# Kernel tuning notes

Hardware: AMD Instinct MI355X
Metric: run time of the kernel (lower is better)

Reference implementation:

```python
import jax, jax.numpy as jnp
from jax import lax
import numpy as np

B = 128          # batch size
S = 207          # input spatial size implied by outputSpatialSize=[8,8]
N_PTS = 256000
NEG = -1e30      # -inf stand-in for masked max-pooling
# BNReLU channel counts in execution order: 8 resnet blocks x (bn1, bn2), final resnet BN(32), last BN(64)
SIZES = [8,8,8,8,8,16,16,16,16,24,24,24,24,32,32,32,32,64]
OFF = np.cumsum([0] + SIZES)

WSHAPES = dict(conv0=(3,3,1,8),
               c1a=(3,3,8,8), c1b=(3,3,8,8), c2a=(3,3,8,8), c2b=(3,3,8,8),
               c3a=(3,3,8,16), c3b=(3,3,16,16), c3r=(3,3,8,16),
               c4a=(3,3,16,16), c4b=(3,3,16,16),
               c5a=(3,3,16,24), c5b=(3,3,24,24), c5r=(3,3,16,24),
               c6a=(3,3,24,24), c6b=(3,3,24,24),
               c7a=(3,3,24,32), c7b=(3,3,32,32), c7r=(3,3,24,32),
               c8a=(3,3,32,32), c8b=(3,3,32,32),
               conv_last=(5,5,32,64))

def _conv(x, w, stride, padding):
    return lax.conv_general_dilated(x, w, (stride, stride), padding,
                                    dimension_numbers=('NHWC', 'HWIO', 'NHWC'))

def _pool_max(x, win, stride, init):
    return lax.reduce_window(x, init, lax.max, (1, win, win, 1), (1, stride, stride, 1), 'VALID')

def _bnrelu(x, m, g, b):
    # eval-mode BN folded to affine, applied on active sites only (inactive stay exactly 0)
    return m * jax.nn.relu(x * g + b)

def _subconv(x, w, m):
    # submanifold conv == dense conv on zero-filled grid, output restricted to active sites
    return _conv(x, w, 1, 'SAME') * m

def _strided(x, w, m, win, stride):
    # scn.Convolution: output site active iff any active input in its receptive field
    m2 = _pool_max(m, win, stride, 0.0)
    return _conv(x, w, stride, 'VALID') * m2, m2

def _block(x, m, g1, b1, w1, g2, b2, w2, wres, stride):
    # pre-activation basic block from scn.SparseResNet
    h = _bnrelu(x, m, g1, b1)
    if stride == 1:
        h, m2 = _subconv(h, w1, m), m
    else:
        h, m2 = _strided(h, w1, m, 3, 2)
    h = _subconv(_bnrelu(h, m2, g2, b2), w2, m2)
    r = x if wres is None else _strided(x, wres, m, 3, 2)[0]
    return h + r, m2

def _forward(locations, batch_idx, features, bn_gamma, bn_beta, W):
    idx = (batch_idx, locations[:, 0], locations[:, 1], jnp.zeros_like(batch_idx))
    x = jnp.zeros((B, S, S, 1), jnp.float32).at[idx].add(features[:, 0])  # InputLayer (sum dups)
    m = jnp.zeros((B, S, S, 1), jnp.float32).at[idx].set(1.0)             # active-site mask
    g = [bn_gamma[OFF[i]:OFF[i+1]] for i in range(len(SIZES))]
    b = [bn_beta[OFF[i]:OFF[i+1]] for i in range(len(SIZES))]
    x = _subconv(x, W['conv0'], m)                              # 1->8 @ 207x207
    # MaxPooling(pool 3, stride 2) over active sites only
    m2 = _pool_max(m, 3, 2, 0.0)
    x = jnp.where(m2 > 0, _pool_max(jnp.where(m > 0, x, NEG), 3, 2, NEG), 0.0)
    m = m2                                                      # @ 103x103
    blocks = [('c1a', 'c1b', None, 1), ('c2a', 'c2b', None, 1),
              ('c3a', 'c3b', 'c3r', 2), ('c4a', 'c4b', None, 1),
              ('c5a', 'c5b', 'c5r', 2), ('c6a', 'c6b', None, 1),
              ('c7a', 'c7b', 'c7r', 2), ('c8a', 'c8b', None, 1)]
    for i, (k1, k2, kr, st) in enumerate(blocks):
        x, m = _block(x, m, g[2*i], b[2*i], W[k1], g[2*i+1], b[2*i+1], W[k2],
                      None if kr is None else W[kr], st)        # 103->51->25->12
    x = _bnrelu(x, m, g[16], b[16])                             # final resnet BNReLU(32)
    x, m = _strided(x, W['conv_last'], m, 5, 1)                 # 32->64, 12x12 -> 8x8
    x = _bnrelu(x, m, g[17], b[17])
    flat = x.transpose(0, 3, 1, 2).reshape(B, -1)               # SparseToDense + flatten (NCHW order)
    return (flat @ W['w_lin'].T).reshape(B, -1, 1)              # [B, 100, 1]

def setup_inputs():
    key = jax.random.key(0)
    ks = iter(jax.random.split(key, 64))
    inp = {
        'locations': jax.random.randint(next(ks), (N_PTS, 2), 0, S, dtype=jnp.int32),
        'batch_idx': jax.random.randint(next(ks), (N_PTS,), 0, B, dtype=jnp.int32),
        'features': jax.random.normal(next(ks), (N_PTS, 1), jnp.float32),
        'bn_gamma': 1.0 + 0.1 * jax.random.normal(next(ks), (int(OFF[-1]),), jnp.float32),
        'bn_beta': 0.1 * jax.random.normal(next(ks), (int(OFF[-1]),), jnp.float32),
    }
    for name, shp in WSHAPES.items():
        fan_in = int(np.prod(shp[:-1]))
        inp[name] = jax.random.normal(next(ks), shp, jnp.float32) * (2.0 / fan_in) ** 0.5
    inp['w_lin'] = jax.random.normal(next(ks), (100, 64 * 8 * 8), jnp.float32) * (1.0 / 4096.0) ** 0.5
    return inp

def reference(locations, batch_idx, features, bn_gamma, bn_beta, conv0,
              c1a, c1b, c2a, c2b, c3a, c3b, c3r, c4a, c4b, c5a, c5b, c5r,
              c6a, c6b, c7a, c7b, c7r, c8a, c8b, conv_last, w_lin):
    W = dict(conv0=conv0, c1a=c1a, c1b=c1b, c2a=c2a, c2b=c2b, c3a=c3a, c3b=c3b, c3r=c3r,
             c4a=c4a, c4b=c4b, c5a=c5a, c5b=c5b, c5r=c5r, c6a=c6a, c6b=c6b,
             c7a=c7a, c7b=c7b, c7r=c7r, c8a=c8a, c8b=c8b, conv_last=conv_last, w_lin=w_lin)
    return _forward(locations, batch_idx, features, bn_gamma, bn_beta, W)
```

## Files before the change

### kernel.cpp

```cpp
#include <hip/hip_runtime.h>

#define S 207
#define BATCH 128
#define NPTS 256000

static const int OFFS[19] = {0,8,16,24,32,40,56,72,88,104,128,152,176,200,232,264,296,328,392};

__global__ void zero2_kernel(float4* __restrict__ a, float4* __restrict__ b, int n4) {
    int i = blockIdx.x * blockDim.x + threadIdx.x;
    if (i < n4) { a[i] = make_float4(0,0,0,0); b[i] = make_float4(0,0,0,0); }
}

__global__ void zero_kernel(float* __restrict__ p, int n) {
    int i = blockIdx.x * blockDim.x + threadIdx.x;
    if (i < n) p[i] = 0.0f;
}

__global__ void scatter_kernel(const int* __restrict__ loc, const int* __restrict__ bidx,
                               const float* __restrict__ feat,
                               float* __restrict__ xs, float* __restrict__ ms) {
    int t = blockIdx.x * blockDim.x + threadIdx.x;
    if (t >= NPTS) return;
    int b = bidx[t];
    int r = loc[2 * t];
    int c = loc[2 * t + 1];
    int idx = (b * S + r) * S + c;
    atomicAdd(&xs[idx], feat[t]);
    ms[idx] = 1.0f;
}

__global__ __launch_bounds__(256) void conv0_pool_kernel(
    const float* __restrict__ xs, const float* __restrict__ ms,
    const float* __restrict__ w,
    float* __restrict__ x1, float* __restrict__ m1) {
    const int Hout = 103;
    int opix = blockIdx.x * 256 + threadIdx.x;
    int total = BATCH * Hout * Hout;
    if (opix >= total) return;
    int wo = opix % Hout;
    int t = opix / Hout;
    int ho = t % Hout;
    int b  = t / Hout;

    float mv[3][3];
    float mwin = 0.0f;
    #pragma unroll
    for (int pi = 0; pi < 3; ++pi)
        #pragma unroll
        for (int pj = 0; pj < 3; ++pj) {
            float m = ms[(b * S + 2 * ho + pi) * S + 2 * wo + pj];
            mv[pi][pj] = m;
            mwin = fmaxf(mwin, m);
        }
    float* xp = x1 + (size_t)opix * 8;
    if (mwin <= 0.0f) {
        *(float4*)xp = make_float4(0,0,0,0);
        *(float4*)(xp + 4) = make_float4(0,0,0,0);
        m1[opix] = 0.0f;
        return;
    }
    float p[5][5];
    #pragma unroll
    for (int r = 0; r < 5; ++r) {
        int ii = 2 * ho - 1 + r;
        #pragma unroll
        for (int c = 0; c < 5; ++c) {
            int jj = 2 * wo - 1 + c;
            bool ok = ((unsigned)ii < (unsigned)S) && ((unsigned)jj < (unsigned)S);
            p[r][c] = ok ? xs[(b * S + ii) * S + jj] : 0.0f;
        }
    }
    float best[8];
    #pragma unroll
    for (int co = 0; co < 8; ++co) best[co] = -1e30f;
    #pragma unroll
    for (int pi = 0; pi < 3; ++pi)
        #pragma unroll
        for (int pj = 0; pj < 3; ++pj) {
            if (mv[pi][pj] > 0.0f) {
                float acc[8];
                #pragma unroll
                for (int co = 0; co < 8; ++co) acc[co] = 0.0f;
                #pragma unroll
                for (int kh = 0; kh < 3; ++kh)
                    #pragma unroll
                    for (int kw = 0; kw < 3; ++kw) {
                        float x = p[pi + kh][pj + kw];
                        #pragma unroll
                        for (int co = 0; co < 8; ++co)
                            acc[co] = fmaf(x, w[(kh * 3 + kw) * 8 + co], acc[co]);
                    }
                #pragma unroll
                for (int co = 0; co < 8; ++co) best[co] = fmaxf(best[co], acc[co]);
            }
        }
    *(float4*)xp = make_float4(best[0], best[1], best[2], best[3]);
    *(float4*)(xp + 4) = make_float4(best[4], best[5], best[6], best[7]);
    m1[opix] = 1.0f;
}

template <int C, int TILE, int NTX>
__global__ __launch_bounds__(256) void resblock_kernel(
    const float* __restrict__ in, const float* __restrict__ mask,
    const float* __restrict__ w1, const float* __restrict__ w2,
    const float* __restrict__ g1, const float* __restrict__ bb1,
    const float* __restrict__ g2, const float* __restrict__ bb2,
    float* __restrict__ out, int H) {
    constexpr int XT = TILE + 4, HT = TILE + 2;
    constexpr int XA = XT * XT, HA = HT * HT;
    __shared__ float xs[C][XA];
    __shared__ float h1[C][HA];
    __shared__ float msh[XA];

    int tid = threadIdx.x;
    int bid = blockIdx.x;
    int b = bid / (NTX * NTX);
    int t = bid % (NTX * NTX);
    int r0 = (t / NTX) * TILE, c0 = (t % NTX) * TILE;

    float gr[C], br[C];
    #pragma unroll
    for (int c = 0; c < C; ++c) { gr[c] = g1[c]; br[c] = bb1[c]; }

    for (int i = tid; i < XA; i += 256) {
        int py = i / XT, px = i % XT;
        int gy = r0 - 2 + py, gx = c0 - 2 + px;
        bool ok = (unsigned)gy < (unsigned)H && (unsigned)gx < (unsigned)H;
        float m = 0.0f;
        if (ok) m = mask[(size_t)(b * H + gy) * H + gx];
        msh[i] = m;
        if (m > 0.0f) {
            const float* ip = in + ((size_t)(b * H + gy) * H + gx) * C;
            #pragma unroll
            for (int c = 0; c < C; ++c)
                xs[c][i] = m * fmaxf(fmaf(ip[c], gr[c], br[c]), 0.0f);
        } else {
            #pragma unroll
            for (int c = 0; c < C; ++c) xs[c][i] = 0.0f;
        }
    }
    #pragma unroll
    for (int c = 0; c < C; ++c) { gr[c] = g2[c]; br[c] = bb2[c]; }
    __syncthreads();

    for (int pos = tid; pos < HA; pos += 256) {
        int py = pos / HT, px = pos % HT;
        float mc = msh[(py + 1) * XT + px + 1];
        float acc[C];
        #pragma unroll
        for (int co = 0; co < C; ++co) acc[co] = 0.0f;
        if (mc > 0.0f) {
            #pragma unroll
            for (int kh = 0; kh < 3; ++kh)
                #pragma unroll
                for (int kw = 0; kw < 3; ++kw) {
                    int pix = (py + kh) * XT + px + kw;
                    const float* wp = w1 + (kh * 3 + kw) * C * C;
                    #pragma unroll
                    for (int ci = 0; ci < C; ++ci) {
                        float xv = xs[ci][pix];
                        #pragma unroll
                        for (int co = 0; co < C; ++co)
                            acc[co] = fmaf(xv, wp[ci * C + co], acc[co]);
                    }
                }
        }
        #pragma unroll
        for (int co = 0; co < C; ++co)
            h1[co][pos] = mc * fmaxf(fmaf(acc[co] * mc, gr[co], br[co]), 0.0f);
    }
    __syncthreads();

    {
        int ty = tid / TILE, tx = tid % TILE;
        int gy = r0 + ty, gx = c0 + tx;
        if (gy < H && gx < H) {
            float mo = msh[(ty + 2) * XT + tx + 2];
            float acc[C];
            #pragma unroll
            for (int co = 0; co < C; ++co) acc[co] = 0.0f;
            if (mo > 0.0f) {
                #pragma unroll
                for (int kh = 0; kh < 3; ++kh)
                    #pragma unroll
                    for (int kw = 0; kw < 3; ++kw) {
                        int pix = (ty + kh) * HT + tx + kw;
                        const float* wp = w2 + (kh * 3 + kw) * C * C;
                        #pragma unroll
                        for (int ci = 0; ci < C; ++ci) {
                            float xv = h1[ci][pix];
                            #pragma unroll
                            for (int co = 0; co < C; ++co)
                                acc[co] = fmaf(xv, wp[ci * C + co], acc[co]);
                        }
                    }
            }
            const float* rp = in + ((size_t)(b * H + gy) * H + gx) * C;
            float* op = out + ((size_t)(b * H + gy) * H + gx) * C;
            #pragma unroll
            for (int j = 0; j < C; j += 4) {
                float4 r4 = *(const float4*)(rp + j);
                float4 o4;
                o4.x = fmaf(acc[j],     mo, r4.x);
                o4.y = fmaf(acc[j + 1], mo, r4.y);
                o4.z = fmaf(acc[j + 2], mo, r4.z);
                o4.w = fmaf(acc[j + 3], mo, r4.w);
                *(float4*)(op + j) = o4;
            }
        }
    }
}

template <int K, int CIN, int COUT, int COT, bool BN, bool RES>
__global__ __launch_bounds__(256) void fconv_kernel(
    const float* __restrict__ in, const float* __restrict__ w,
    const float* __restrict__ g, const float* __restrict__ bbn,
    const float* __restrict__ mIn, const float* __restrict__ mOut,
    const float* __restrict__ res, float* __restrict__ out,
    int Hin, int Hout, int stride, int pad) {
    const int Win = Hin, Wout = Hout;
    int npix = BATCH * Hout * Wout;
    int opix = blockIdx.x * 256 + threadIdx.x;
    if (opix >= npix) return;
    int co0 = blockIdx.y * COT;
    int wo = opix % Wout;
    int t = opix / Wout;
    int ho = t % Hout;
    int b  = t / Hout;

    float mo = mOut[opix];
    float* op = out + (size_t)opix * COUT + co0;
    if (mo <= 0.0f) {
        #pragma unroll
        for (int j = 0; j < COT; j += 4) {
            float4 r4 = RES ? *(const float4*)(res + (size_t)opix * COUT + co0 + j)
                            : make_float4(0,0,0,0);
            *(float4*)(op + j) = r4;
        }
        return;
    }
    float acc[COT];
    #pragma unroll
    for (int j = 0; j < COT; ++j) acc[j] = 0.0f;

    #pragma unroll
    for (int kh = 0; kh < K; ++kh) {
        int ih = ho * stride + kh - pad;
        if ((unsigned)ih >= (unsigned)Hin) continue;
        #pragma unroll
        for (int kw = 0; kw < K; ++kw) {
            int iw = wo * stride + kw - pad;
            if ((unsigned)iw >= (unsigned)Win) continue;
            int ipix = (b * Hin + ih) * Win + iw;
            float mi = 1.0f;
            if (BN) { mi = mIn[ipix]; if (mi <= 0.0f) continue; }
            const float* ip = in + (size_t)ipix * CIN;
            const float* wp = w + (kh * K + kw) * CIN * COUT + co0;
            #pragma unroll
            for (int ci = 0; ci < CIN; ci += 4) {
                float4 xv = *(const float4*)(ip + ci);
                if (BN) {
                    xv.x = mi * fmaxf(fmaf(xv.x, g[ci],     bbn[ci]),     0.0f);
                    xv.y = mi * fmaxf(fmaf(xv.y, g[ci + 1], bbn[ci + 1]), 0.0f);
                    xv.z = mi * fmaxf(fmaf(xv.z, g[ci + 2], bbn[ci + 2]), 0.0f);
                    xv.w = mi * fmaxf(fmaf(xv.w, g[ci + 3], bbn[ci + 3]), 0.0f);
                }
                #pragma unroll
                for (int j = 0; j < COT; ++j) {
                    acc[j] = fmaf(xv.x, wp[(ci    ) * COUT + j], acc[j]);
                    acc[j] = fmaf(xv.y, wp[(ci + 1) * COUT + j], acc[j]);
                    acc[j] = fmaf(xv.z, wp[(ci + 2) * COUT + j], acc[j]);
                    acc[j] = fmaf(xv.w, wp[(ci + 3) * COUT + j], acc[j]);
                }
            }
        }
    }
    #pragma unroll
    for (int j = 0; j < COT; j += 4) {
        float4 o4;
        o4.x = acc[j] * mo; o4.y = acc[j+1] * mo; o4.z = acc[j+2] * mo; o4.w = acc[j+3] * mo;
        if (RES) {
            float4 r4 = *(const float4*)(res + (size_t)opix * COUT + co0 + j);
            o4.x += r4.x; o4.y += r4.y; o4.z += r4.z; o4.w += r4.w;
        }
        *(float4*)(op + j) = o4;
    }
}

template <int CIN, int COUT, int COT>
__global__ __launch_bounds__(256) void strided_ra_kernel(
    const float* __restrict__ in,
    const float* __restrict__ wR, const float* __restrict__ wA,
    const float* __restrict__ g, const float* __restrict__ bbn,
    const float* __restrict__ mIn, float* __restrict__ mOutBuf,
    float* __restrict__ outR, float* __restrict__ outA,
    int Hin, int Hout) {
    constexpr int NG = COUT / COT;
    int npix = BATCH * Hout * Hout;
    int opix = blockIdx.x * 256 + threadIdx.x;
    if (opix >= npix) return;
    int path = blockIdx.y / NG;
    int co0  = (blockIdx.y % NG) * COT;
    int wo = opix % Hout;
    int t = opix / Hout;
    int ho = t % Hout;
    int b  = t / Hout;

    const float* wsel = path ? wA : wR;
    float acc[COT];
    #pragma unroll
    for (int j = 0; j < COT; ++j) acc[j] = 0.0f;
    float m2 = 0.0f;

    #pragma unroll
    for (int kh = 0; kh < 3; ++kh) {
        int ih = 2 * ho + kh;
        #pragma unroll
        for (int kw = 0; kw < 3; ++kw) {
            int iw = 2 * wo + kw;
            int ipix = (b * Hin + ih) * Hin + iw;
            float mi = mIn[ipix];
            if (mi <= 0.0f) continue;
            m2 = fmaxf(m2, mi);
            const float* ip = in + (size_t)ipix * CIN;
            const float* wp = wsel + (kh * 3 + kw) * CIN * COUT + co0;
            #pragma unroll
            for (int ci = 0; ci < CIN; ci += 4) {
                float4 xv = *(const float4*)(ip + ci);
                if (path) {
                    xv.x = mi * fmaxf(fmaf(xv.x, g[ci],     bbn[ci]),     0.0f);
                    xv.y = mi * fmaxf(fmaf(xv.y, g[ci + 1], bbn[ci + 1]), 0.0f);
                    xv.z = mi * fmaxf(fmaf(xv.z, g[ci + 2], bbn[ci + 2]), 0.0f);
                    xv.w = mi * fmaxf(fmaf(xv.w, g[ci + 3], bbn[ci + 3]), 0.0f);
                }
                #pragma unroll
                for (int j = 0; j < COT; ++j) {
                    acc[j] = fmaf(xv.x, wp[(ci    ) * COUT + j], acc[j]);
                    acc[j] = fmaf(xv.y, wp[(ci + 1) * COUT + j], acc[j]);
                    acc[j] = fmaf(xv.z, wp[(ci + 2) * COUT + j], acc[j]);
                    acc[j] = fmaf(xv.w, wp[(ci + 3) * COUT + j], acc[j]);
                }
            }
        }
    }
    if (blockIdx.y == 0) mOutBuf[opix] = m2;
    float* op = (path ? outA : outR) + (size_t)opix * COUT + co0;
    #pragma unroll
    for (int j = 0; j < COT; j += 4) {
        float4 o4;
        o4.x = acc[j] * m2; o4.y = acc[j+1] * m2; o4.z = acc[j+2] * m2; o4.w = acc[j+3] * m2;
        *(float4*)(op + j) = o4;
    }
}

__global__ __launch_bounds__(256) void convlast_kernel(
    const float* __restrict__ in,
    const float* __restrict__ w,
    const float* __restrict__ g, const float* __restrict__ bb,
    const float* __restrict__ mIn,
    float* __restrict__ part) {
    __shared__ float xs[32 * 97];
    __shared__ float ws[5 * 32 * 64];
    int b   = blockIdx.x;
    int kh  = blockIdx.y;
    int tid = threadIdx.x;
    for (int i = tid; i < 8 * 12 * 32; i += 256) {
        int ci = i & 31;
        int p  = i >> 5;
        int gpix = (b * 12 + kh + p / 12) * 12 + (p % 12);
        float m = mIn[gpix];
        float v = 0.0f;
        if (m > 0.0f) v = fmaxf(fmaf(in[(size_t)gpix * 32 + ci], g[ci], bb[ci]), 0.0f);
        xs[ci * 97 + p] = v;
    }
    {
        const float4* src = (const float4*)(w + kh * (5 * 32 * 64));
        float4* dst = (float4*)ws;
        for (int i = tid; i < 5 * 32 * 64 / 4; i += 256) dst[i] = src[i];
    }
    __syncthreads();

    int px = tid & 63;
    int cg = tid >> 6;
    int ho = px >> 3, wo = px & 7;
    float acc[16];
    #pragma unroll
    for (int j = 0; j < 16; ++j) acc[j] = 0.0f;
    #pragma unroll
    for (int kw = 0; kw < 5; ++kw) {
        const float* xp = xs + ho * 12 + wo + kw;
        const float* wp = ws + kw * (32 * 64) + cg * 16;
        #pragma unroll
        for (int ci = 0; ci < 32; ++ci) {
            float xv = xp[ci * 97];
            const float* wr = wp + ci * 64;
            #pragma unroll
            for (int j = 0; j < 16; j += 4) {
                float4 w4 = *(const float4*)(wr + j);
                acc[j]     = fmaf(xv, w4.x, acc[j]);
                acc[j + 1] = fmaf(xv, w4.y, acc[j + 1]);
                acc[j + 2] = fmaf(xv, w4.z, acc[j + 2]);
                acc[j + 3] = fmaf(xv, w4.w, acc[j + 3]);
            }
        }
    }
    float* op = part + ((((size_t)kh * BATCH + b) * 64 + px) * 64) + cg * 16;
    #pragma unroll
    for (int j = 0; j < 16; j += 4)
        *(float4*)(op + j) = make_float4(acc[j], acc[j+1], acc[j+2], acc[j+3]);
}

__global__ __launch_bounds__(256) void bn_tr_kernel(
    const float* __restrict__ part, const float* __restrict__ m,
    const float* __restrict__ g, const float* __restrict__ bb,
    float* __restrict__ xt) {
    int tid = blockIdx.x * 256 + threadIdx.x;
    if (tid >= BATCH * 4096) return;
    int c = tid & 63, hw = (tid >> 6) & 63, b = tid >> 12;
    float s = 0.0f;
    #pragma unroll
    for (int k = 0; k < 5; ++k)
        s += part[(((size_t)k * BATCH + b) * 64 + hw) * 64 + c];
    float v = m[b * 64 + hw] * fmaxf(fmaf(s, g[c], bb[c]), 0.0f);
    xt[((size_t)b << 12) + c * 64 + hw] = v;
}

__global__ void pool_kernel(const float* __restrict__ in, float* __restrict__ out,
                            int Hin, int Win, int Hout, int Wout, int win, int stride) {
    int tid = blockIdx.x * blockDim.x + threadIdx.x;
    int total = BATCH * Hout * Wout;
    if (tid >= total) return;
    int wo = tid % Wout;
    int p = tid / Wout;
    int ho = p % Hout;
    int b  = p / Hout;
    float mx = 0.0f;
    for (int i = 0; i < win; ++i)
        for (int j = 0; j < win; ++j)
            mx = fmaxf(mx, in[(b * Hin + ho * stride + i) * Win + wo * stride + j]);
    out[tid] = mx;
}

__global__ __launch_bounds__(256) void linear_gemm_kernel(
    const float* __restrict__ xt, const float* __restrict__ wl,
    float* __restrict__ out) {
    int o = blockIdx.x;
    int half = threadIdx.x >> 7;
    int b = threadIdx.x & 127;
    int k0 = blockIdx.y * 512 + half * 256;
    const float* xp = xt + ((size_t)b << 12) + k0;
    const float* wp = wl + o * 4096 + k0;
    float acc = 0.0f;
    #pragma unroll 16
    for (int k = 0; k < 256; k += 4) {
        float4 xv = *(const float4*)(xp + k);
        float4 wv = *(const float4*)(wp + k);
        acc = fmaf(xv.x, wv.x, acc); acc = fmaf(xv.y, wv.y, acc);
        acc = fmaf(xv.z, wv.z, acc); acc = fmaf(xv.w, wv.w, acc);
    }
    atomicAdd(&out[b * 100 + o], acc);
}

template <int K, int CIN, int COUT, int COT, bool BN, bool RES>
static inline void fconv(hipStream_t s, const float* in, const float* w,
                         const float* g, const float* bbn,
                         const float* mIn, const float* mOut, const float* res,
                         float* out, int Hin, int Hout, int stride, int pad) {
    int npix = BATCH * Hout * Hout;
    dim3 grid((npix + 255) / 256, COUT / COT);
    fconv_kernel<K, CIN, COUT, COT, BN, RES><<<grid, 256, 0, s>>>(
        in, w, g, bbn, mIn, mOut, res, out, Hin, Hout, stride, pad);
}

template <int CIN, int COUT, int COT>
static inline void strided_ra(hipStream_t s, const float* in, const float* wR, const float* wA,
                              const float* g, const float* bbn, const float* mIn,
                              float* mOutBuf, float* outR, float* outA, int Hin, int Hout) {
    int npix = BATCH * Hout * Hout;
    dim3 grid((npix + 255) / 256, 2 * (COUT / COT));
    strided_ra_kernel<CIN, COUT, COT><<<grid, 256, 0, s>>>(
        in, wR, wA, g, bbn, mIn, mOutBuf, outR, outA, Hin, Hout);
}

extern "C" void kernel_launch(void* const* d_in, const int* in_sizes, int n_in,
                              void* d_out, int out_size, void* d_ws, size_t ws_size,
                              hipStream_t stream) {
    const int*   loc   = (const int*)d_in[0];
    const int*   bidx  = (const int*)d_in[1];
    const float* feat  = (const float*)d_in[2];
    const float* gamma = (const float*)d_in[3];
    const float* beta  = (const float*)d_in[4];
    const float* Wconv0 = (const float*)d_in[5];
    const float* Wc1a = (const float*)d_in[6];
    const float* Wc1b = (const float*)d_in[7];
    const float* Wc2a = (const float*)d_in[8];
    const float* Wc2b = (const float*)d_in[9];
    const float* Wc3a = (const float*)d_in[10];
    const float* Wc3b = (const float*)d_in[11];
    const float* Wc3r = (const float*)d_in[12];
    const float* Wc4a = (const float*)d_in[13];
    const float* Wc4b = (const float*)d_in[14];
    const float* Wc5a = (const float*)d_in[15];
    const float* Wc5b = (const float*)d_in[16];
    const float* Wc5r = (const float*)d_in[17];
    const float* Wc6a = (const float*)d_in[18];
    const float* Wc6b = (const float*)d_in[19];
    const float* Wc7a = (const float*)d_in[20];
    const float* Wc7b = (const float*)d_in[21];
    const float* Wc7r = (const float*)d_in[22];
    const float* Wc8a = (const float*)d_in[23];
    const float* Wc8b = (const float*)d_in[24];
    const float* Wlast = (const float*)d_in[25];
    const float* wlin  = (const float*)d_in[26];

    const size_t SZB = (size_t)BATCH * 103 * 103 * 8;
    const size_t SZM = (size_t)BATCH * 103 * 103;
    float* b0 = (float*)d_ws;
    float* b1 = b0 + SZB;
    float* b2 = b1 + SZB;
    float* m0 = b2 + SZB;
    float* m1 = m0 + SZM;

    const float* G[18];
    const float* Bt[18];
    for (int i = 0; i < 18; ++i) { G[i] = gamma + OFFS[i]; Bt[i] = beta + OFFS[i]; }

    {
        int n = BATCH * S * S;
        zero2_kernel<<<(n / 4 + 255) / 256, 256, 0, stream>>>((float4*)b1, (float4*)b2, n / 4);
        scatter_kernel<<<(NPTS + 255) / 256, 256, 0, stream>>>(loc, bidx, feat, b1, b2);
        int total = BATCH * 103 * 103;
        conv0_pool_kernel<<<(total + 255) / 256, 256, 0, stream>>>(b1, b2, Wconv0, b0, m0);
    }

    resblock_kernel<8, 16, 7><<<dim3(7 * 7 * BATCH), 256, 0, stream>>>(
        b0, m0, Wc1a, Wc1b, G[0], Bt[0], G[1], Bt[1], b1, 103);
    resblock_kernel<8, 16, 7><<<dim3(7 * 7 * BATCH), 256, 0, stream>>>(
        b1, m0, Wc2a, Wc2b, G[2], Bt[2], G[3], Bt[3], b2, 103);
    strided_ra<8, 16, 16>(stream, b2, Wc3r, Wc3a, G[4], Bt[4], m0, m1, b0, b1, 103, 51);
    fconv<3, 16, 16, 8, true, true >(stream, b1, Wc3b, G[5], Bt[5], m1, m1, b0, b2, 51, 51, 1, 1);
    fconv<3, 16, 16, 8, true, false>(stream, b2, Wc4a, G[6], Bt[6], m1, m1, nullptr, b0, 51, 51, 1, 1);
    fconv<3, 16, 16, 8, true, true >(stream, b0, Wc4b, G[7], Bt[7], m1, m1, b2,      b1, 51, 51, 1, 1);
    strided_ra<16, 24, 24>(stream, b1, Wc5r, Wc5a, G[8], Bt[8], m1, m0, b0, b2, 51, 25);
    fconv<3, 24, 24, 8, true, true >(stream, b2, Wc5b, G[9], Bt[9], m0, m0, b0, b1, 25, 25, 1, 1);
    fconv<3, 24, 24, 8, true, false>(stream, b1, Wc6a, G[10], Bt[10], m0, m0, nullptr, b0, 25, 25, 1, 1);
    fconv<3, 24, 24, 8, true, true >(stream, b0, Wc6b, G[11], Bt[11], m0, m0, b1,      b2, 25, 25, 1, 1);
    strided_ra<24, 32, 8>(stream, b2, Wc7r, Wc7a, G[12], Bt[12], m0, m1, b0, b1, 25, 12);
    fconv<3, 32, 32, 4, true, true >(stream, b1, Wc7b, G[13], Bt[13], m1, m1, b0, b2, 12, 12, 1, 1);
    fconv<3, 32, 32, 4, true, false>(stream, b2, Wc8a, G[14], Bt[14], m1, m1, nullptr, b0, 12, 12, 1, 1);
    fconv<3, 32, 32, 4, true, true >(stream, b0, Wc8b, G[15], Bt[15], m1, m1, b2,      b1, 12, 12, 1, 1);
    pool_kernel<<<(BATCH * 64 + 255) / 256, 256, 0, stream>>>(m1, m0, 12, 12, 8, 8, 5, 1);
    convlast_kernel<<<dim3(BATCH, 5), 256, 0, stream>>>(b1, Wlast, G[16], Bt[16], m1, b0);
    bn_tr_kernel<<<(BATCH * 4096 + 255) / 256, 256, 0, stream>>>(b0, m0, G[17], Bt[17], b2);
    zero_kernel<<<(BATCH * 100 + 255) / 256, 256, 0, stream>>>((float*)d_out, BATCH * 100);
    linear_gemm_kernel<<<dim3(100, 8), 256, 0, stream>>>(b2, wlin, (float*)d_out);
}
```

Measured before the change: 766.2 us.

## Fuse blocks 4 and 6 into resblock kernel and merge strided residual/main paths

Replaces the two back-to-back fconv launches of resnet blocks 4 and 6 with the fused tiled resblock kernel, generalized so a tile can exceed 256 output pixels and the input load uses float4 vectors. Strided downsample kernels now compute residual and main paths in one thread, reading each input pixel and mask once instead of twice. This removes intermediate global writes and reads, and some launches, at the cost of more registers per thread and fewer blocks.

```diff
diff --git a/kernel.cpp b/kernel.cpp
--- a/kernel.cpp
+++ b/kernel.cpp
@@ -132,8 +132,13 @@
         if (m > 0.0f) {
             const float* ip = in + ((size_t)(b * H + gy) * H + gx) * C;
             #pragma unroll
-            for (int c = 0; c < C; ++c)
-                xs[c][i] = m * fmaxf(fmaf(ip[c], gr[c], br[c]), 0.0f);
+            for (int c = 0; c < C; c += 4) {
+                float4 x4 = *(const float4*)(ip + c);
+                xs[c    ][i] = m * fmaxf(fmaf(x4.x, gr[c],     br[c]),     0.0f);
+                xs[c + 1][i] = m * fmaxf(fmaf(x4.y, gr[c + 1], br[c + 1]), 0.0f);
+                xs[c + 2][i] = m * fmaxf(fmaf(x4.z, gr[c + 2], br[c + 2]), 0.0f);
+                xs[c + 3][i] = m * fmaxf(fmaf(x4.w, gr[c + 3], br[c + 3]), 0.0f);
+            }
         } else {
             #pragma unroll
             for (int c = 0; c < C; ++c) xs[c][i] = 0.0f;
@@ -171,8 +176,8 @@
     }
     __syncthreads();
 
-    {
-        int ty = tid / TILE, tx = tid % TILE;
+    for (int pos = tid; pos < TILE * TILE; pos += 256) {
+        int ty = pos / TILE, tx = pos % TILE;
         int gy = r0 + ty, gx = c0 + tx;
         if (gy < H && gx < H) {
             float mo = msh[(ty + 2) * XT + tx + 2];
@@ -288,28 +293,25 @@
 }
 
 template <int CIN, int COUT, int COT>
-__global__ __launch_bounds__(256) void strided_ra_kernel(
+__global__ __launch_bounds__(256) void strided_both_kernel(
     const float* __restrict__ in,
     const float* __restrict__ wR, const float* __restrict__ wA,
     const float* __restrict__ g, const float* __restrict__ bbn,
     const float* __restrict__ mIn, float* __restrict__ mOutBuf,
     float* __restrict__ outR, float* __restrict__ outA,
     int Hin, int Hout) {
-    constexpr int NG = COUT / COT;
     int npix = BATCH * Hout * Hout;
     int opix = blockIdx.x * 256 + threadIdx.x;
     if (opix >= npix) return;
-    int path = blockIdx.y / NG;
-    int co0  = (blockIdx.y % NG) * COT;
+    int co0 = blockIdx.y * COT;
     int wo = opix % Hout;
     int t = opix / Hout;
     int ho = t % Hout;
     int b  = t / Hout;
 
-    const float* wsel = path ? wA : wR;
-    float acc[COT];
-    #pragma unroll
-    for (int j = 0; j < COT; ++j) acc[j] = 0.0f;
+    float accR[COT], accA[COT];
+    #pragma unroll
+    for (int j = 0; j < COT; ++j) { accR[j] = 0.0f; accA[j] = 0.0f; }
     float m2 = 0.0f;
 
     #pragma unroll
@@ -322,34 +324,38 @@
             float mi = mIn[ipix];
             if (mi <= 0.0f) continue;
             m2 = fmaxf(m2, mi);
-            const float* ip = in + (size_t)ipix * CIN;
-            const float* wp = wsel + (kh * 3 + kw) * CIN * COUT + co0;
+            const float* ip  = in + (size_t)ipix * CIN;
+            const float* wpR = wR + (kh * 3 + kw) * CIN * COUT + co0;
+            const float* wpA = wA + (kh * 3 + kw) * CIN * COUT + co0;
             #pragma unroll
             for (int ci = 0; ci < CIN; ci += 4) {
                 float4 xv = *(const float4*)(ip + ci);
-                if (path) {
-                    xv.x = mi * fmaxf(fmaf(xv.x, g[ci],     bbn[ci]),     0.0f);
-                    xv.y = mi * fmaxf(fmaf(xv.y, g[ci + 1], bbn[ci + 1]), 0.0f);
-                    xv.z = mi * fmaxf(fmaf(xv.z, g[ci + 2], bbn[ci + 2]), 0.0f);
-                    xv.w = mi * fmaxf(fmaf(xv.w, g[ci + 3], bbn[ci + 3]), 0.0f);
+                float4 xa;
+                xa.x = mi * fmaxf(fmaf(xv.x, g[ci],     bbn[ci]),     0.0f);
+                xa.y = mi * fmaxf(fmaf(xv.y, g[ci + 1], bbn[ci + 1]), 0.0f);
+                xa.z = mi * fmaxf(fmaf(xv.z, g[ci + 2], bbn[ci + 2]), 0.0f);
+                xa.w = mi * fmaxf(fmaf(xv.w, g[ci + 3], bbn[ci + 3]), 0.0f);
+                #pragma unroll
+                for (int j = 0; j < COT; ++j) {
+                    accR[j] = fmaf(xv.x, wpR[(ci    ) * COUT + j], accR[j]);
+                    accR[j] = fmaf(xv.y, wpR[(ci + 1) * COUT + j], accR[j]);
+                    accR[j] = fmaf(xv.z, wpR[(ci + 2) * COUT + j], accR[j]);
+                    accR[j] = fmaf(xv.w, wpR[(ci + 3) * COUT + j], accR[j]);
+                    accA[j] = fmaf(xa.x, wpA[(ci    ) * COUT + j], accA[j]);
+                    accA[j] = fmaf(xa.y, wpA[(ci + 1) * COUT + j], accA[j]);
+                    accA[j] = fmaf(xa.z, wpA[(ci + 2) * COUT + j], accA[j]);
+                    accA[j] = fmaf(xa.w, wpA[(ci + 3) * COUT + j], accA[j]);
                 }
-                #pragma unroll
-                for (int j = 0; j < COT; ++j) {
-                    acc[j] = fmaf(xv.x, wp[(ci    ) * COUT + j], acc[j]);
-                    acc[j] = fmaf(xv.y, wp[(ci + 1) * COUT + j], acc[j]);
-                    acc[j] = fmaf(xv.z, wp[(ci + 2) * COUT + j], acc[j]);
-                    acc[j] = fmaf(xv.w, wp[(ci + 3) * COUT + j], acc[j]);
-                }
             }
         }
     }
     if (blockIdx.y == 0) mOutBuf[opix] = m2;
-    float* op = (path ? outA : outR) + (size_t)opix * COUT + co0;
+    float* opR = outR + (size_t)opix * COUT + co0;
+    float* opA = outA + (size_t)opix * COUT + co0;
     #pragma unroll
     for (int j = 0; j < COT; j += 4) {
-        float4 o4;
-        o4.x = acc[j] * m2; o4.y = acc[j+1] * m2; o4.z = acc[j+2] * m2; o4.w = acc[j+3] * m2;
-        *(float4*)(op + j) = o4;
+        *(float4*)(opR + j) = make_float4(accR[j] * m2, accR[j+1] * m2, accR[j+2] * m2, accR[j+3] * m2);
+        *(float4*)(opA + j) = make_float4(accA[j] * m2, accA[j+1] * m2, accA[j+2] * m2, accA[j+3] * m2);
     }
 }
 
@@ -473,12 +479,12 @@
 }
 
 template <int CIN, int COUT, int COT>
-static inline void strided_ra(hipStream_t s, const float* in, const float* wR, const float* wA,
-                              const float* g, const float* bbn, const float* mIn,
-                              float* mOutBuf, float* outR, float* outA, int Hin, int Hout) {
+static inline void strided_both(hipStream_t s, const float* in, const float* wR, const float* wA,
+                                const float* g, const float* bbn, const float* mIn,
+                                float* mOutBuf, float* outR, float* outA, int Hin, int Hout) {
     int npix = BATCH * Hout * Hout;
-    dim3 grid((npix + 255) / 256, 2 * (COUT / COT));
-    strided_ra_kernel<CIN, COUT, COT><<<grid, 256, 0, s>>>(
+    dim3 grid((npix + 255) / 256, COUT / COT);
+    strided_both_kernel<CIN, COUT, COT><<<grid, 256, 0, s>>>(
         in, wR, wA, g, bbn, mIn, mOutBuf, outR, outA, Hin, Hout);
 }
 
@@ -537,15 +543,15 @@
         b0, m0, Wc1a, Wc1b, G[0], Bt[0], G[1], Bt[1], b1, 103);
     resblock_kernel<8, 16, 7><<<dim3(7 * 7 * BATCH), 256, 0, stream>>>(
         b1, m0, Wc2a, Wc2b, G[2], Bt[2], G[3], Bt[3], b2, 103);
-    strided_ra<8, 16, 16>(stream, b2, Wc3r, Wc3a, G[4], Bt[4], m0, m1, b0, b1, 103, 51);
+    strided_both<8, 16, 16>(stream, b2, Wc3r, Wc3a, G[4], Bt[4], m0, m1, b0, b1, 103, 51);
     fconv<3, 16, 16, 8, true, true >(stream, b1, Wc3b, G[5], Bt[5], m1, m1, b0, b2, 51, 51, 1, 1);
-    fconv<3, 16, 16, 8, true, false>(stream, b2, Wc4a, G[6], Bt[6], m1, m1, nullptr, b0, 51, 51, 1, 1);
-    fconv<3, 16, 16, 8, true, true >(stream, b0, Wc4b, G[7], Bt[7], m1, m1, b2,      b1, 51, 51, 1, 1);
-    strided_ra<16, 24, 24>(stream, b1, Wc5r, Wc5a, G[8], Bt[8], m1, m0, b0, b2, 51, 25);
+    resblock_kernel<16, 16, 4><<<dim3(4 * 4 * BATCH), 256, 0, stream>>>(
+        b2, m1, Wc4a, Wc4b, G[6], Bt[6], G[7], Bt[7], b1, 51);
+    strided_both<16, 24, 12>(stream, b1, Wc5r, Wc5a, G[8], Bt[8], m1, m0, b0, b2, 51, 25);
     fconv<3, 24, 24, 8, true, true >(stream, b2, Wc5b, G[9], Bt[9], m0, m0, b0, b1, 25, 25, 1, 1);
-    fconv<3, 24, 24, 8, true, false>(stream, b1, Wc6a, G[10], Bt[10], m0, m0, nullptr, b0, 25, 25, 1, 1);
-    fconv<3, 24, 24, 8, true, true >(stream, b0, Wc6b, G[11], Bt[11], m0, m0, b1,      b2, 25, 25, 1, 1);
-    strided_ra<24, 32, 8>(stream, b2, Wc7r, Wc7a, G[12], Bt[12], m0, m1, b0, b1, 25, 12);
+    resblock_kernel<24, 13, 2><<<dim3(2 * 2 * BATCH), 256, 0, stream>>>(
+        b1, m0, Wc6a, Wc6b, G[10], Bt[10], G[11], Bt[11], b2, 25);
+    strided_both<24, 32, 8>(stream, b2, Wc7r, Wc7a, G[12], Bt[12], m0, m1, b0, b1, 25, 12);
     fconv<3, 32, 32, 4, true, true >(stream, b1, Wc7b, G[13], Bt[13], m1, m1, b0, b2, 12, 12, 1, 1);
     fconv<3, 32, 32, 4, true, false>(stream, b2, Wc8a, G[14], Bt[14], m1, m1, nullptr, b0, 12, 12, 1, 1);
     fconv<3, 32, 32, 4, true, true >(stream, b0, Wc8b, G[15], Bt[15], m1, m1, b2,      b1, 12, 12, 1, 1);
```

New measurement: 1.074 ms. +40.2%, slower.
